# Performance work log

Hardware: AMD Instinct MI355X
Metric: run time of the kernel (lower is better)

## Reference

```python
import jax, jax.numpy as jnp
import numpy as np

HIDDEN = 1024
HEADS = 16
HEAD_DIM = HIDDEN // HEADS
GAMMA = 0.5
B, S = 2, 2048


def setup_inputs() -> dict:
    key = jax.random.key(0)
    ks = jax.random.split(key, 9)
    sc = 1.0 / np.sqrt(HIDDEN)
    x = jax.random.normal(ks[0], (B, S, HIDDEN), dtype=jnp.float32)
    attn_mask = jnp.zeros((S, S), dtype=bool)  # True = masked; all-False here
    Wq = jax.random.normal(ks[1], (HIDDEN, HIDDEN), dtype=jnp.float32) * sc
    bq = jnp.zeros((HIDDEN,), dtype=jnp.float32)
    Wk = jax.random.normal(ks[2], (HIDDEN, HIDDEN), dtype=jnp.float32) * sc
    bk = jnp.zeros((HIDDEN,), dtype=jnp.float32)
    Wv = jax.random.normal(ks[3], (HIDDEN, HIDDEN), dtype=jnp.float32) * sc
    bv = jnp.zeros((HIDDEN,), dtype=jnp.float32)
    Wo = jax.random.normal(ks[4], (HIDDEN, HIDDEN), dtype=jnp.float32) * sc
    bo = jnp.zeros((HIDDEN,), dtype=jnp.float32)
    return {"x": x, "attn_mask": attn_mask, "Wq": Wq, "bq": bq,
            "Wk": Wk, "bk": bk, "Wv": Wv, "bv": bv, "Wo": Wo, "bo": bo}


def reference(x, attn_mask, Wq, bq, Wk, bk, Wv, bv, Wo, bo):
    Bn, Sn, _ = x.shape
    # projections (torch Linear: x @ W.T + b), reshape to [B, H, S, Dh]
    def proj(W, b):
        y = x @ W.T + b
        return y.reshape(Bn, Sn, HEADS, HEAD_DIM).transpose(0, 2, 1, 3)
    q, k, v = proj(Wq, bq), proj(Wk, bk), proj(Wv, bv)
    scores = jnp.einsum('bhqd,bhkd->bhqk', q, k) / np.sqrt(HEAD_DIM)
    # diversity bias: cosine similarity of raw x (F.normalize eps=1e-12)
    normed = x / jnp.maximum(jnp.linalg.norm(x, axis=-1, keepdims=True), 1e-12)
    sim = jnp.einsum('bqd,bkd->bqk', normed, normed)
    scores = scores - GAMMA * sim[:, None, :, :]
    scores = jnp.where(attn_mask[None, None, :, :], -jnp.inf, scores)
    probs = jax.nn.softmax(scores, axis=-1)
    ctx = jnp.einsum('bhqk,bhkd->bhqd', probs, v)
    ctx = ctx.transpose(0, 2, 1, 3).reshape(Bn, Sn, HIDDEN)
    return ctx @ Wo.T + bo
```

## Files before the change

### kernel.cpp

```cpp
#include <hip/hip_runtime.h>

#define HID 1024
#define SEQ 2048
#define NB 2
#define NH 16
#define HD 64

#define C1 0.1803368801111204f
#define C2 0.7213475204444817f

typedef __attribute__((ext_vector_type(8))) short bf16x8;
typedef __attribute__((ext_vector_type(8))) unsigned short u16x8;
typedef __attribute__((ext_vector_type(4))) float f32x4;

__device__ __forceinline__ unsigned short f2bf(float f) {
  unsigned u = __builtin_bit_cast(unsigned, f);
  u += 0x7fffu + ((u >> 16) & 1u);
  return (unsigned short)(u >> 16);
}
__device__ __forceinline__ float bf2f(unsigned short u) {
  return __builtin_bit_cast(float, ((unsigned)u) << 16);
}

#define GLOAD16(gsrc, ldst)                                                     \
  __builtin_amdgcn_global_load_lds(                                             \
      (const __attribute__((address_space(1))) void*)(gsrc),                    \
      (__attribute__((address_space(3))) void*)(ldst), 16, 0, 0)

__global__ __launch_bounds__(256) void convert_w_kernel(
    const float* __restrict__ Wq, const float* __restrict__ Wk,
    const float* __restrict__ Wv, const float* __restrict__ Wo,
    unsigned short* __restrict__ Wb) {
  int i = blockIdx.x * 256 + threadIdx.x;
  const int per = (HID * HID) / 8;
  int m = i / per;
  const float* sp = (m == 0) ? Wq : (m == 1) ? Wk : (m == 2) ? Wv : Wo;
  int j = (i - m * per) * 8;
  const float4* p = reinterpret_cast<const float4*>(sp + j);
  float4 a = p[0], b = p[1];
  u16x8 o;
  o[0] = f2bf(a.x); o[1] = f2bf(a.y); o[2] = f2bf(a.z); o[3] = f2bf(a.w);
  o[4] = f2bf(b.x); o[5] = f2bf(b.y); o[6] = f2bf(b.z); o[7] = f2bf(b.w);
  *reinterpret_cast<u16x8*>(Wb + (size_t)i * 8) = o;
}

__global__ __launch_bounds__(256) void rownorm_kernel(
    const float* __restrict__ x, unsigned short* __restrict__ xb,
    unsigned short* __restrict__ nxb) {
  int row = blockIdx.x, tid = threadIdx.x;
  const float4 v = reinterpret_cast<const float4*>(x + (size_t)row * HID)[tid];
  float ss = v.x * v.x + v.y * v.y + v.z * v.z + v.w * v.w;
#pragma unroll
  for (int off = 32; off; off >>= 1) ss += __shfl_xor(ss, off, 64);
  __shared__ float wsum[4];
  if ((tid & 63) == 0) wsum[tid >> 6] = ss;
  __syncthreads();
  float tot = wsum[0] + wsum[1] + wsum[2] + wsum[3];
  float inv = 1.0f / fmaxf(sqrtf(tot), 1e-12f);
  ushort4 a, b;
  a.x = f2bf(v.x); a.y = f2bf(v.y); a.z = f2bf(v.z); a.w = f2bf(v.w);
  b.x = f2bf(v.x * inv); b.y = f2bf(v.y * inv);
  b.z = f2bf(v.z * inv); b.w = f2bf(v.w * inv);
  reinterpret_cast<ushort4*>(xb  + (size_t)row * HID)[tid] = a;
  reinterpret_cast<ushort4*>(nxb + (size_t)row * HID)[tid] = b;
}

template <int MODE>
__global__ __launch_bounds__(256) void gemm_nt(
    const unsigned short* __restrict__ A, long strideA,
    const unsigned short* __restrict__ B, long strideB,
    void* __restrict__ Cv, long strideC, int ldc,
    int M, int N, int K,
    const float* __restrict__ b0, const float* __restrict__ b1,
    const float* __restrict__ b2, const unsigned char* __restrict__ mask) {
  __shared__ __align__(16) unsigned short As[128 * 32];
  __shared__ __align__(16) unsigned short Bs[128 * 32];
  int tid = threadIdx.x, lane = tid & 63, wid = tid >> 6;
  int g = lane >> 4, lr = lane & 15;
  int wr = wid >> 1, wc = wid & 1;
  int m0 = blockIdx.y * 128, n0 = blockIdx.x * 128;
  const unsigned short* Ab = A + (size_t)blockIdx.z * strideA
      + (size_t)(m0 + wid * 32 + (lane >> 2)) * K + (lane & 3) * 8;
  const unsigned short* Bb = B + (size_t)blockIdx.z * strideB
      + (size_t)(n0 + wid * 32 + (lane >> 2)) * K + (lane & 3) * 8;
  unsigned short* la = As + wid * 1024;
  unsigned short* lb = Bs + wid * 1024;
  f32x4 acc[4][4] = {};
  for (int k0 = 0; k0 < K; k0 += 32) {
    GLOAD16(Ab + k0, la);
    GLOAD16(Ab + 16 * K + k0, la + 512);
    GLOAD16(Bb + k0, lb);
    GLOAD16(Bb + 16 * K + k0, lb + 512);
    __syncthreads();
    bf16x8 af[4], bfr[4];
#pragma unroll
    for (int i = 0; i < 4; i++) {
      af[i]  = *reinterpret_cast<const bf16x8*>(&As[(wr * 64 + i * 16 + lr) * 32 + g * 8]);
      bfr[i] = *reinterpret_cast<const bf16x8*>(&Bs[(wc * 64 + i * 16 + lr) * 32 + g * 8]);
    }
#pragma unroll
    for (int i = 0; i < 4; i++)
#pragma unroll
      for (int j = 0; j < 4; j++)
        acc[i][j] = __builtin_amdgcn_mfma_f32_16x16x32_bf16(af[i], bfr[j], acc[i][j], 0, 0, 0);
    __syncthreads();
  }
#pragma unroll
  for (int i = 0; i < 4; i++)
#pragma unroll
    for (int j = 0; j < 4; j++) {
      int col = n0 + wc * 64 + j * 16 + lr;
#pragma unroll
      for (int r = 0; r < 4; r++) {
        int row = m0 + wr * 64 + i * 16 + 4 * g + r;
        float v = acc[i][j][r];
        if (MODE == 0) {
          const float* bp = (col < 1024) ? b0 : b1;
          v += bp[col & 1023];
          ((unsigned short*)Cv)[(size_t)blockIdx.z * strideC + (size_t)row * ldc + col] = f2bf(v);
        } else if (MODE == 1) {
          float t = -C2 * v + (mask[(size_t)row * N + col] ? -1e30f : 0.0f);
          ((unsigned short*)Cv)[(size_t)blockIdx.z * strideC + (size_t)row * ldc + col] = f2bf(t);
        } else if (MODE == 2) {
          v += b0[col];
          ((float*)Cv)[(size_t)blockIdx.z * strideC + (size_t)row * ldc + col] = v;
        } else {
          v += b0[row];
          ((unsigned short*)Cv)[(size_t)blockIdx.z * strideC + (size_t)row * ldc + col] = f2bf(v);
        }
      }
    }
}

__global__ __launch_bounds__(256, 4) void flash_kernel(
    const unsigned short* __restrict__ QK,
    const unsigned short* __restrict__ VT,
    const unsigned short* __restrict__ D2,
    unsigned short* __restrict__ ctxb) {
  int h = blockIdx.x, qt = blockIdx.y, b = blockIdx.z;
  int tid = threadIdx.x, wid = tid >> 6, lane = tid & 63;
  int g = lane >> 4, lr = lane & 15;
  __shared__ __align__(16) unsigned short Ks[2][64 * 64];
  __shared__ __align__(16) unsigned short Vt[2][64 * 64];
  const size_t ld = 2 * HID;
  const size_t bS = (size_t)b * SEQ;
  const int qbase = qt * 64 + wid * 16;

  const unsigned short* qp = QK + (bS + qbase + lr) * ld + h * HD + g * 8;
  bf16x8 qf0 = *reinterpret_cast<const bf16x8*>(qp);
  bf16x8 qf1 = *reinterpret_cast<const bf16x8*>(qp + 32);

  const int p0 = wid * 16 + (lane >> 3);
  const int key0 = ((p0 >> 5) & 1) * 32 + (((p0 >> 2) & 3) << 3)
                 + ((p0 >> 4) & 1) * 4 + (p0 & 3);
  const unsigned short* gK0 = QK + (bS + key0) * ld + HID + h * HD
                              + (((lane & 7) ^ (lane >> 3)) << 3);
  const unsigned short* gK1 = gK0 + 16 * ld;

  const unsigned short* gV0 = VT + (size_t)(h * HD + wid * 16 + (lane >> 3)) * (2 * SEQ)
                              + bS + (((lane & 7) ^ (lane >> 3)) << 3);
  const unsigned short* gV1 = gV0 + (size_t)8 * (2 * SEQ);

  const unsigned short* bD = D2 + (size_t)b * SEQ * SEQ
                             + (size_t)(qbase + lr) * SEQ + 8 * g;

  GLOAD16(gK0, &Ks[0][wid * 1024]);
  GLOAD16(gK1, &Ks[0][wid * 1024 + 512]);
  GLOAD16(gV0, &Vt[0][wid * 1024]);
  GLOAD16(gV1, &Vt[0][wid * 1024 + 512]);
  ushort4 bvc[4];
  bvc[0] = *reinterpret_cast<const ushort4*>(bD + 0);
  bvc[1] = *reinterpret_cast<const ushort4*>(bD + 4);
  bvc[2] = *reinterpret_cast<const ushort4*>(bD + 32);
  bvc[3] = *reinterpret_cast<const ushort4*>(bD + 36);
  __syncthreads();

  f32x4 acc[4] = {};
  f32x4 rsacc = {};
  const int kb0 = lr * 64 + ((g ^ (lr & 7)) << 3);
  bf16x8 ones;
#pragma unroll
  for (int i = 0; i < 8; i++) ones[i] = 0x3F80;

  for (int kt = 0; kt < 32; ++kt) {
    const int cb = kt & 1;
    const unsigned short* ks = &Ks[cb][0];
    const unsigned short* vt = &Vt[cb][0];
    ushort4 bvn[4];
    if (kt < 31) {
      GLOAD16(gK0 + (size_t)(kt + 1) * 64 * ld, &Ks[cb ^ 1][wid * 1024]);
      GLOAD16(gK1 + (size_t)(kt + 1) * 64 * ld, &Ks[cb ^ 1][wid * 1024 + 512]);
      GLOAD16(gV0 + (kt + 1) * 64, &Vt[cb ^ 1][wid * 1024]);
      GLOAD16(gV1 + (kt + 1) * 64, &Vt[cb ^ 1][wid * 1024 + 512]);
      const unsigned short* bn = bD + (kt + 1) * 64;
      bvn[0] = *reinterpret_cast<const ushort4*>(bn + 0);
      bvn[1] = *reinterpret_cast<const ushort4*>(bn + 4);
      bvn[2] = *reinterpret_cast<const ushort4*>(bn + 32);
      bvn[3] = *reinterpret_cast<const ushort4*>(bn + 36);
    }

    f32x4 s[4];
    __builtin_amdgcn_s_setprio(1);
#pragma unroll
    for (int kc = 0; kc < 4; kc++) {
      bf16x8 kf0 = *reinterpret_cast<const bf16x8*>(ks + kc * 1024 + kb0);
      bf16x8 kf1 = *reinterpret_cast<const bf16x8*>(ks + kc * 1024 + (kb0 ^ 32));
      f32x4 z = {};
      z = __builtin_amdgcn_mfma_f32_16x16x32_bf16(kf0, qf0, z, 0, 0, 0);
      s[kc] = __builtin_amdgcn_mfma_f32_16x16x32_bf16(kf1, qf1, z, 0, 0, 0);
    }
    __builtin_amdgcn_s_setprio(0);

    bf16x8 pa[2];
#pragma unroll
    for (int c2 = 0; c2 < 2; c2++) {
      float p0f = exp2f(fmaf(s[2 * c2][0], C1, bf2f(bvc[2 * c2].x)));
      float p1f = exp2f(fmaf(s[2 * c2][1], C1, bf2f(bvc[2 * c2].y)));
      float p2f = exp2f(fmaf(s[2 * c2][2], C1, bf2f(bvc[2 * c2].z)));
      float p3f = exp2f(fmaf(s[2 * c2][3], C1, bf2f(bvc[2 * c2].w)));
      float p4f = exp2f(fmaf(s[2 * c2 + 1][0], C1, bf2f(bvc[2 * c2 + 1].x)));
      float p5f = exp2f(fmaf(s[2 * c2 + 1][1], C1, bf2f(bvc[2 * c2 + 1].y)));
      float p6f = exp2f(fmaf(s[2 * c2 + 1][2], C1, bf2f(bvc[2 * c2 + 1].z)));
      float p7f = exp2f(fmaf(s[2 * c2 + 1][3], C1, bf2f(bvc[2 * c2 + 1].w)));
      uint4 W;
      W.x = __builtin_amdgcn_perm(__builtin_bit_cast(unsigned, p1f),
                                  __builtin_bit_cast(unsigned, p0f), 0x07060302u);
      W.y = __builtin_amdgcn_perm(__builtin_bit_cast(unsigned, p3f),
                                  __builtin_bit_cast(unsigned, p2f), 0x07060302u);
      W.z = __builtin_amdgcn_perm(__builtin_bit_cast(unsigned, p5f),
                                  __builtin_bit_cast(unsigned, p4f), 0x07060302u);
      W.w = __builtin_amdgcn_perm(__builtin_bit_cast(unsigned, p7f),
                                  __builtin_bit_cast(unsigned, p6f), 0x07060302u);
      pa[c2] = __builtin_bit_cast(bf16x8, W);
    }

    __builtin_amdgcn_s_setprio(1);
#pragma unroll
    for (int c2 = 0; c2 < 2; c2++) {
      rsacc = __builtin_amdgcn_mfma_f32_16x16x32_bf16(pa[c2], ones, rsacc, 0, 0, 0);
#pragma unroll
      for (int df = 0; df < 4; df++) {
        bf16x8 vf = *reinterpret_cast<const bf16x8*>(
            vt + (df * 16 + lr) * 64 + (((4 * c2 + g) ^ (lr & 7)) << 3));
        acc[df] = __builtin_amdgcn_mfma_f32_16x16x32_bf16(pa[c2], vf, acc[df], 0, 0, 0);
      }
    }
    __builtin_amdgcn_s_setprio(0);

    if (kt < 31) {
      bvc[0] = bvn[0]; bvc[1] = bvn[1]; bvc[2] = bvn[2]; bvc[3] = bvn[3];
    }
    __syncthreads();
  }
  float l0 = 1.0f / rsacc[0], l1 = 1.0f / rsacc[1];
  float l2 = 1.0f / rsacc[2], l3 = 1.0f / rsacc[3];
  unsigned short* op = ctxb + (bS + qbase + 4 * g) * HID + h * HD + lr;
#pragma unroll
  for (int df = 0; df < 4; df++) {
    op[0 * HID + df * 16] = f2bf(acc[df][0] * l0);
    op[1 * HID + df * 16] = f2bf(acc[df][1] * l1);
    op[2 * HID + df * 16] = f2bf(acc[df][2] * l2);
    op[3 * HID + df * 16] = f2bf(acc[df][3] * l3);
  }
}

extern "C" void kernel_launch(void* const* d_in, const int* in_sizes, int n_in,
                              void* d_out, int out_size, void* d_ws, size_t ws_size,
                              hipStream_t stream) {
  const float* x = (const float*)d_in[0];
  const unsigned char* mask = (const unsigned char*)d_in[1];
  const float* Wq = (const float*)d_in[2];
  const float* bq = (const float*)d_in[3];
  const float* Wk = (const float*)d_in[4];
  const float* bk = (const float*)d_in[5];
  const float* Wv = (const float*)d_in[6];
  const float* bv = (const float*)d_in[7];
  const float* Wo = (const float*)d_in[8];
  const float* bo = (const float*)d_in[9];
  float* out = (float*)d_out;

  char* ws = (char*)d_ws;
  const size_t MiB = 1024 * 1024;
  unsigned short* xb  = (unsigned short*)(ws + 0 * MiB);
  unsigned short* nxb = (unsigned short*)(ws + 8 * MiB);
  unsigned short* Wb  = (unsigned short*)(ws + 16 * MiB);
  unsigned short* QK  = (unsigned short*)(ws + 24 * MiB);
  unsigned short* VT  = (unsigned short*)(ws + 40 * MiB);
  unsigned short* D2  = (unsigned short*)(ws + 48 * MiB);
  unsigned short* ctx = (unsigned short*)(ws + 64 * MiB);

  convert_w_kernel<<<2048, 256, 0, stream>>>(Wq, Wk, Wv, Wo, Wb);
  rownorm_kernel<<<NB * SEQ, 256, 0, stream>>>(x, xb, nxb);
  gemm_nt<0><<<dim3(16, 32, 1), 256, 0, stream>>>(
      xb, 0, Wb, 0, QK, 0, 2 * HID, NB * SEQ, 2 * HID, HID, bq, bk, nullptr, nullptr);
  gemm_nt<3><<<dim3(32, 8, 1), 256, 0, stream>>>(
      Wb + (size_t)2 * HID * HID, 0, xb, 0, VT, 0, 2 * SEQ, HID, NB * SEQ, HID,
      bv, nullptr, nullptr, nullptr);
  gemm_nt<1><<<dim3(16, 16, 2), 256, 0, stream>>>(
      nxb, (long)SEQ * HID, nxb, (long)SEQ * HID, D2, (long)SEQ * SEQ, SEQ,
      SEQ, SEQ, HID, nullptr, nullptr, nullptr, mask);
  flash_kernel<<<dim3(NH, SEQ / 64, NB), 256, 0, stream>>>(QK, VT, D2, ctx);
  gemm_nt<2><<<dim3(8, 32, 1), 256, 0, stream>>>(
      ctx, 0, Wb + (size_t)3 * HID * HID, 0, out, 0, HID, NB * SEQ, HID, HID,
      bo, nullptr, nullptr, nullptr);
}
```

Before: 204.2 us.

## Merge prep kernels, fuse projection and similarity GEMMs, exploit similarity symmetry

```diff
diff --git a/kernel.cpp b/kernel.cpp
--- a/kernel.cpp
+++ b/kernel.cpp
@@ -27,62 +27,82 @@
       (const __attribute__((address_space(1))) void*)(gsrc),                    \
       (__attribute__((address_space(3))) void*)(ldst), 16, 0, 0)
 
-__global__ __launch_bounds__(256) void convert_w_kernel(
+__global__ __launch_bounds__(256) void prep_kernel(
+    const float* __restrict__ x,
     const float* __restrict__ Wq, const float* __restrict__ Wk,
     const float* __restrict__ Wv, const float* __restrict__ Wo,
-    unsigned short* __restrict__ Wb) {
-  int i = blockIdx.x * 256 + threadIdx.x;
-  const int per = (HID * HID) / 8;
-  int m = i / per;
-  const float* sp = (m == 0) ? Wq : (m == 1) ? Wk : (m == 2) ? Wv : Wo;
-  int j = (i - m * per) * 8;
-  const float4* p = reinterpret_cast<const float4*>(sp + j);
-  float4 a = p[0], b = p[1];
-  u16x8 o;
-  o[0] = f2bf(a.x); o[1] = f2bf(a.y); o[2] = f2bf(a.z); o[3] = f2bf(a.w);
-  o[4] = f2bf(b.x); o[5] = f2bf(b.y); o[6] = f2bf(b.z); o[7] = f2bf(b.w);
-  *reinterpret_cast<u16x8*>(Wb + (size_t)i * 8) = o;
-}
-
-__global__ __launch_bounds__(256) void rownorm_kernel(
-    const float* __restrict__ x, unsigned short* __restrict__ xb,
-    unsigned short* __restrict__ nxb) {
-  int row = blockIdx.x, tid = threadIdx.x;
-  const float4 v = reinterpret_cast<const float4*>(x + (size_t)row * HID)[tid];
-  float ss = v.x * v.x + v.y * v.y + v.z * v.z + v.w * v.w;
-#pragma unroll
-  for (int off = 32; off; off >>= 1) ss += __shfl_xor(ss, off, 64);
-  __shared__ float wsum[4];
-  if ((tid & 63) == 0) wsum[tid >> 6] = ss;
-  __syncthreads();
-  float tot = wsum[0] + wsum[1] + wsum[2] + wsum[3];
-  float inv = 1.0f / fmaxf(sqrtf(tot), 1e-12f);
-  ushort4 a, b;
-  a.x = f2bf(v.x); a.y = f2bf(v.y); a.z = f2bf(v.z); a.w = f2bf(v.w);
-  b.x = f2bf(v.x * inv); b.y = f2bf(v.y * inv);
-  b.z = f2bf(v.z * inv); b.w = f2bf(v.w * inv);
-  reinterpret_cast<ushort4*>(xb  + (size_t)row * HID)[tid] = a;
-  reinterpret_cast<ushort4*>(nxb + (size_t)row * HID)[tid] = b;
-}
-
-template <int MODE>
-__global__ __launch_bounds__(256) void gemm_nt(
-    const unsigned short* __restrict__ A, long strideA,
-    const unsigned short* __restrict__ B, long strideB,
-    void* __restrict__ Cv, long strideC, int ldc,
-    int M, int N, int K,
-    const float* __restrict__ b0, const float* __restrict__ b1,
-    const float* __restrict__ b2, const unsigned char* __restrict__ mask) {
+    unsigned short* __restrict__ Wb,
+    unsigned short* __restrict__ xb, unsigned short* __restrict__ nxb) {
+  int tid = threadIdx.x;
+  if (blockIdx.x < 2048) {
+    int i = blockIdx.x * 256 + tid;
+    const int per = (HID * HID) / 8;
+    int m = i / per;
+    const float* sp = (m == 0) ? Wq : (m == 1) ? Wk : (m == 2) ? Wv : Wo;
+    int j = (i - m * per) * 8;
+    const float4* p = reinterpret_cast<const float4*>(sp + j);
+    float4 a = p[0], b = p[1];
+    u16x8 o;
+    o[0] = f2bf(a.x); o[1] = f2bf(a.y); o[2] = f2bf(a.z); o[3] = f2bf(a.w);
+    o[4] = f2bf(b.x); o[5] = f2bf(b.y); o[6] = f2bf(b.z); o[7] = f2bf(b.w);
+    *reinterpret_cast<u16x8*>(Wb + (size_t)i * 8) = o;
+  } else {
+    int row = blockIdx.x - 2048;
+    const float4 v = reinterpret_cast<const float4*>(x + (size_t)row * HID)[tid];
+    float ss = v.x * v.x + v.y * v.y + v.z * v.z + v.w * v.w;
+#pragma unroll
+    for (int off = 32; off; off >>= 1) ss += __shfl_xor(ss, off, 64);
+    __shared__ float wsum[4];
+    if ((tid & 63) == 0) wsum[tid >> 6] = ss;
+    __syncthreads();
+    float tot = wsum[0] + wsum[1] + wsum[2] + wsum[3];
+    float inv = 1.0f / fmaxf(sqrtf(tot), 1e-12f);
+    ushort4 a, b;
+    a.x = f2bf(v.x); a.y = f2bf(v.y); a.z = f2bf(v.z); a.w = f2bf(v.w);
+    b.x = f2bf(v.x * inv); b.y = f2bf(v.y * inv);
+    b.z = f2bf(v.z * inv); b.w = f2bf(v.w * inv);
+    reinterpret_cast<ushort4*>(xb  + (size_t)row * HID)[tid] = a;
+    reinterpret_cast<ushort4*>(nxb + (size_t)row * HID)[tid] = b;
+  }
+}
+
+__global__ __launch_bounds__(256) void mega_gemm(
+    const unsigned short* __restrict__ xb, const unsigned short* __restrict__ nxb,
+    const unsigned short* __restrict__ Wb,
+    unsigned short* __restrict__ QK, unsigned short* __restrict__ VT,
+    unsigned short* __restrict__ D2,
+    const float* __restrict__ bq, const float* __restrict__ bk,
+    const float* __restrict__ bv, const unsigned char* __restrict__ mask) {
+  const int K = HID;
+  int bid = blockIdx.x;
+  int mode, m0, n0;
+  const unsigned short *A, *B;
+  size_t zoff = 0;
+  if (bid < 512) {
+    mode = 0; m0 = (bid >> 4) * 128; n0 = (bid & 15) * 128;
+    A = xb; B = Wb;
+  } else if (bid < 768) {
+    mode = 3; int t = bid - 512; m0 = (t >> 5) * 128; n0 = (t & 31) * 128;
+    A = Wb + (size_t)2 * HID * HID; B = xb;
+  } else {
+    mode = 1; int t = bid - 768; int z = 0;
+    if (t >= 136) { z = 1; t -= 136; }
+    int a = (int)((sqrtf(8.0f * t + 1.0f) - 1.0f) * 0.5f);
+    while (a * (a + 1) / 2 > t) a--;
+    while ((a + 1) * (a + 2) / 2 <= t) a++;
+    int bI = t - a * (a + 1) / 2;
+    m0 = bI * 128; n0 = a * 128;
+    A = nxb + (size_t)z * SEQ * HID; B = A;
+    zoff = (size_t)z * SEQ * SEQ;
+  }
+
   __shared__ __align__(16) unsigned short As[128 * 32];
   __shared__ __align__(16) unsigned short Bs[128 * 32];
   int tid = threadIdx.x, lane = tid & 63, wid = tid >> 6;
   int g = lane >> 4, lr = lane & 15;
   int wr = wid >> 1, wc = wid & 1;
-  int m0 = blockIdx.y * 128, n0 = blockIdx.x * 128;
-  const unsigned short* Ab = A + (size_t)blockIdx.z * strideA
-      + (size_t)(m0 + wid * 32 + (lane >> 2)) * K + (lane & 3) * 8;
-  const unsigned short* Bb = B + (size_t)blockIdx.z * strideB
-      + (size_t)(n0 + wid * 32 + (lane >> 2)) * K + (lane & 3) * 8;
+  const unsigned short* Ab = A + (size_t)(m0 + wid * 32 + (lane >> 2)) * K + (lane & 3) * 8;
+  const unsigned short* Bb = B + (size_t)(n0 + wid * 32 + (lane >> 2)) * K + (lane & 3) * 8;
   unsigned short* la = As + wid * 1024;
   unsigned short* lb = Bs + wid * 1024;
   f32x4 acc[4][4] = {};
@@ -114,20 +134,66 @@
       for (int r = 0; r < 4; r++) {
         int row = m0 + wr * 64 + i * 16 + 4 * g + r;
         float v = acc[i][j][r];
-        if (MODE == 0) {
-          const float* bp = (col < 1024) ? b0 : b1;
-          v += bp[col & 1023];
-          ((unsigned short*)Cv)[(size_t)blockIdx.z * strideC + (size_t)row * ldc + col] = f2bf(v);
-        } else if (MODE == 1) {
-          float t = -C2 * v + (mask[(size_t)row * N + col] ? -1e30f : 0.0f);
-          ((unsigned short*)Cv)[(size_t)blockIdx.z * strideC + (size_t)row * ldc + col] = f2bf(t);
-        } else if (MODE == 2) {
-          v += b0[col];
-          ((float*)Cv)[(size_t)blockIdx.z * strideC + (size_t)row * ldc + col] = v;
+        if (mode == 0) {
+          const float* bp = (col < 1024) ? bq : bk;
+          QK[(size_t)row * 2048 + col] = f2bf(v + bp[col & 1023]);
+        } else if (mode == 3) {
+          VT[(size_t)row * 4096 + col] = f2bf(v + bv[row]);
         } else {
-          v += b0[row];
-          ((unsigned short*)Cv)[(size_t)blockIdx.z * strideC + (size_t)row * ldc + col] = f2bf(v);
+          float t1 = -C2 * v + (mask[(size_t)row * SEQ + col] ? -1e30f : 0.0f);
+          D2[zoff + (size_t)row * SEQ + col] = f2bf(t1);
+          if (m0 != n0) {
+            float t2 = -C2 * v + (mask[(size_t)col * SEQ + row] ? -1e30f : 0.0f);
+            D2[zoff + (size_t)col * SEQ + row] = f2bf(t2);
+          }
         }
+      }
+    }
+}
+
+__global__ __launch_bounds__(256) void gemm_out(
+    const unsigned short* __restrict__ A, const unsigned short* __restrict__ B,
+    float* __restrict__ C, const float* __restrict__ b0) {
+  const int K = HID;
+  __shared__ __align__(16) unsigned short As[128 * 32];
+  __shared__ __align__(16) unsigned short Bs[128 * 32];
+  int tid = threadIdx.x, lane = tid & 63, wid = tid >> 6;
+  int g = lane >> 4, lr = lane & 15;
+  int wr = wid >> 1, wc = wid & 1;
+  int m0 = blockIdx.y * 128, n0 = blockIdx.x * 128;
+  const unsigned short* Ab = A + (size_t)(m0 + wid * 32 + (lane >> 2)) * K + (lane & 3) * 8;
+  const unsigned short* Bb = B + (size_t)(n0 + wid * 32 + (lane >> 2)) * K + (lane & 3) * 8;
+  unsigned short* la = As + wid * 1024;
+  unsigned short* lb = Bs + wid * 1024;
+  f32x4 acc[4][4] = {};
+  for (int k0 = 0; k0 < K; k0 += 32) {
+    GLOAD16(Ab + k0, la);
+    GLOAD16(Ab + 16 * K + k0, la + 512);
+    GLOAD16(Bb + k0, lb);
+    GLOAD16(Bb + 16 * K + k0, lb + 512);
+    __syncthreads();
+    bf16x8 af[4], bfr[4];
+#pragma unroll
+    for (int i = 0; i < 4; i++) {
+      af[i]  = *reinterpret_cast<const bf16x8*>(&As[(wr * 64 + i * 16 + lr) * 32 + g * 8]);
+      bfr[i] = *reinterpret_cast<const bf16x8*>(&Bs[(wc * 64 + i * 16 + lr) * 32 + g * 8]);
+    }
+#pragma unroll
+    for (int i = 0; i < 4; i++)
+#pragma unroll
+      for (int j = 0; j < 4; j++)
+        acc[i][j] = __builtin_amdgcn_mfma_f32_16x16x32_bf16(af[i], bfr[j], acc[i][j], 0, 0, 0);
+    __syncthreads();
+  }
+#pragma unroll
+  for (int i = 0; i < 4; i++)
+#pragma unroll
+    for (int j = 0; j < 4; j++) {
+      int col = n0 + wc * 64 + j * 16 + lr;
+#pragma unroll
+      for (int r = 0; r < 4; r++) {
+        int row = m0 + wr * 64 + i * 16 + 4 * g + r;
+        C[(size_t)row * HID + col] = acc[i][j][r] + b0[col];
       }
     }
 }
@@ -289,18 +355,9 @@
   unsigned short* D2  = (unsigned short*)(ws + 48 * MiB);
   unsigned short* ctx = (unsigned short*)(ws + 64 * MiB);
 
-  convert_w_kernel<<<2048, 256, 0, stream>>>(Wq, Wk, Wv, Wo, Wb);
-  rownorm_kernel<<<NB * SEQ, 256, 0, stream>>>(x, xb, nxb);
-  gemm_nt<0><<<dim3(16, 32, 1), 256, 0, stream>>>(
-      xb, 0, Wb, 0, QK, 0, 2 * HID, NB * SEQ, 2 * HID, HID, bq, bk, nullptr, nullptr);
-  gemm_nt<3><<<dim3(32, 8, 1), 256, 0, stream>>>(
-      Wb + (size_t)2 * HID * HID, 0, xb, 0, VT, 0, 2 * SEQ, HID, NB * SEQ, HID,
-      bv, nullptr, nullptr, nullptr);
-  gemm_nt<1><<<dim3(16, 16, 2), 256, 0, stream>>>(
-      nxb, (long)SEQ * HID, nxb, (long)SEQ * HID, D2, (long)SEQ * SEQ, SEQ,
-      SEQ, SEQ, HID, nullptr, nullptr, nullptr, mask);
+  prep_kernel<<<6144, 256, 0, stream>>>(x, Wq, Wk, Wv, Wo, Wb, xb, nxb);
+  mega_gemm<<<1040, 256, 0, stream>>>(xb, nxb, Wb, QK, VT, D2, bq, bk, bv, mask);
   flash_kernel<<<dim3(NH, SEQ / 64, NB), 256, 0, stream>>>(QK, VT, D2, ctx);
-  gemm_nt<2><<<dim3(8, 32, 1), 256, 0, stream>>>(
-      ctx, 0, Wb + (size_t)3 * HID * HID, 0, out, 0, HID, NB * SEQ, HID, HID,
-      bo, nullptr, nullptr, nullptr);
-}
+  gemm_out<<<dim3(8, 32), 256, 0, stream>>>(
+      ctx, Wb + (size_t)3 * HID * HID, out, bo);
+}
```

Result: faster. 196.3 us (-3.9%).
